# Optimization experiments

Measured on AMD Instinct MI355X. Metric: run time of the kernel, lower is better.

The kernel has to match this reference:

```python
import jax, jax.numpy as jnp
import numpy as np

B, T, C, HS = 256, 256, 384, 64

def setup_inputs() -> dict:
    key = jax.random.key(0)
    k1, k2, k3, k4 = jax.random.split(key, 4)
    s = 1.0 / np.sqrt(C)  # Linear-like init scale
    return {
        "x": jax.random.normal(k1, (B, T, C), dtype=jnp.float32),
        "Wq": jax.random.normal(k2, (C, HS), dtype=jnp.float32) * s,
        "Wk": jax.random.normal(k3, (C, HS), dtype=jnp.float32) * s,
        "Wv": jax.random.normal(k4, (C, HS), dtype=jnp.float32) * s,
    }

def reference(x, Wq, Wk, Wv):
    # q,k,v: [B,T,HS]
    q = jnp.einsum("btc,ch->bth", x, Wq)
    k = jnp.einsum("btc,ch->bth", x, Wk)
    v = jnp.einsum("btc,ch->bth", x, Wv)
    scale = k.shape[-1] ** -0.5
    scores = jnp.einsum("bth,bsh->bts", q, k) * scale  # [B,T,T]
    causal = jnp.tril(jnp.ones((x.shape[1], x.shape[1]), dtype=bool))
    scores = jnp.where(causal, scores, -jnp.inf)
    attn = jax.nn.softmax(scores, axis=-1)
    # dropout omitted (eval mode / deterministic reference)
    return jnp.einsum("bts,bsh->bth", attn, v)
```

## Files before the change

kernel.cpp:

```cpp
#include <hip/hip_runtime.h>
#include <hip/hip_bf16.h>

#define NB 256
#define NT 256
#define NC 384
#define NH 64
#define NW 192
#define WT_ELEMS (NW * NC)

typedef short bf16x8 __attribute__((ext_vector_type(8)));
typedef float f32x4 __attribute__((ext_vector_type(4)));

__device__ __forceinline__ unsigned short f2bf(float f) {
  union { float f; unsigned int i; } c;
  c.f = f;
  const unsigned int r = c.i + 0x7fffu + ((c.i >> 16) & 1u);
  return (unsigned short)(r >> 16);
}

__device__ __forceinline__ unsigned short f2bf_hw(float f) {
  __hip_bfloat16 b = __float2bfloat16(f);
  return *reinterpret_cast<unsigned short*>(&b);
}

__device__ __forceinline__ bf16x8 cvt8(float4 lo, float4 hi) {
  union { bf16x8 v; unsigned short u[8]; } au;
  au.u[0] = f2bf_hw(lo.x); au.u[1] = f2bf_hw(lo.y);
  au.u[2] = f2bf_hw(lo.z); au.u[3] = f2bf_hw(lo.w);
  au.u[4] = f2bf_hw(hi.x); au.u[5] = f2bf_hw(hi.y);
  au.u[6] = f2bf_hw(hi.z); au.u[7] = f2bf_hw(hi.w);
  return au.v;
}

__global__ __launch_bounds__(256) void w_prep_kernel(
    const float* __restrict__ Wq,
    const float* __restrict__ Wk,
    const float* __restrict__ Wv,
    unsigned short* __restrict__ Wt2) {
  const int o = blockIdx.x * 256 + threadIdx.x;
  if (o >= WT_ELEMS) return;
  const int j = o & 7;
  const int lane = (o >> 3) & 63;
  const int fi = o >> 9;
  const int ni = fi % 12;
  const int kt = fi / 12;
  const int n = ni * 16 + (lane & 15);
  const int k = kt * 32 + ((lane >> 4) << 3) + j;
  const float* W = (n < 64) ? Wq : (n < 128) ? Wk : Wv;
  Wt2[o] = f2bf(W[k * NH + (n & 63)]);
}

__global__ __launch_bounds__(1024, 4) void fused_qkv_attn_kernel(
    const float* __restrict__ x,
    const unsigned short* __restrict__ Wt2,
    float* __restrict__ out) {
  __shared__ __align__(16) unsigned char lds[147456];

  const int tid = threadIdx.x;
  const int w = tid >> 6;
  const int lane = tid & 63;
  const int l15 = lane & 15;
  const int lg = lane >> 4;
  const int b = blockIdx.x;
  const int row0 = b * NT;
  const int qt =
      (int)((0x583E2F49C1A7B6D0ull >> (w << 2)) & 15ull);
  const int wbase = qt * 16;

  f32x4 acc[12];
#pragma unroll
  for (int ni = 0; ni < 12; ++ni)
#pragma unroll
    for (int r = 0; r < 4; ++r) acc[ni][r] = 0.f;

#pragma unroll
  for (int i = 0; i < 9; ++i) {
    const int idx = i * 1024 + tid;
    __builtin_amdgcn_global_load_lds(
        (const __attribute__((address_space(1))) void*)(Wt2 + idx * 8),
        (__attribute__((address_space(3))) void*)(lds + idx * 16), 16, 0, 0);
  }

  const float* xa0 = x + (size_t)(row0 + wbase + l15) * NC + lg * 8;

  float4 aA0, aA1, aB0, aB1, aC0, aC1;

#define LOADA(S, KT)                                                          \
  do {                                                                        \
    a##S##0 = *reinterpret_cast<const float4*>(xa0 + (KT)*32);                \
    a##S##1 = *reinterpret_cast<const float4*>(xa0 + (KT)*32 + 4);            \
  } while (0)

  LOADA(A, 0);
  LOADA(B, 1);
  LOADA(C, 2);

  asm volatile("s_waitcnt vmcnt(0)" ::: "memory");
  __builtin_amdgcn_s_barrier();

  const unsigned short* Wl =
      reinterpret_cast<const unsigned short*>(lds) + lane * 8;

#define STEP(S, KT)                                                           \
  do {                                                                        \
    const bf16x8 afr = cvt8(a##S##0, a##S##1);                                \
    if ((KT) + 3 < 12) LOADA(S, (KT) + 3);                                    \
    _Pragma("unroll") for (int ni = 0; ni < 12; ++ni) {                       \
      const bf16x8 bfr = *reinterpret_cast<const bf16x8*>(                    \
          Wl + (size_t)((KT)*12 + ni) * 512);                                 \
      acc[ni] = __builtin_amdgcn_mfma_f32_16x16x32_bf16(                      \
          afr, bfr, acc[ni], 0, 0, 0);                                        \
    }                                                                         \
  } while (0)

  STEP(A, 0);  STEP(B, 1);  STEP(C, 2);
  STEP(A, 3);  STEP(B, 4);  STEP(C, 5);
  STEP(A, 6);  STEP(B, 7);  STEP(C, 8);
  STEP(A, 9);  STEP(B, 10); STEP(C, 11);

  __syncthreads();

  unsigned short* Kls = reinterpret_cast<unsigned short*>(lds);
  unsigned short* Vtls = reinterpret_cast<unsigned short*>(lds + 32768);
  unsigned short* Qls = reinterpret_cast<unsigned short*>(lds + 65536);
  unsigned short* Pls = reinterpret_cast<unsigned short*>(lds + 98304);

#pragma unroll
  for (int ni = 0; ni < 12; ++ni) {
    const int n = ni * 16 + l15;
#pragma unroll
    for (int r = 0; r < 4; ++r) {
      const int srow = wbase + lg * 4 + r;
      const unsigned short val = f2bf_hw(acc[ni][r]);
      if (ni < 4) {
        Qls[srow * 64 + (n ^ ((srow & 7) << 3))] = val;
      } else if (ni < 8) {
        const int h = n - 64;
        Kls[srow * 64 + (h ^ ((srow & 7) << 3))] = val;
      } else {
        const int h = n - 128;
        Vtls[h * 256 + (srow ^ ((h & 7) << 3))] = val;
      }
    }
  }
  __syncthreads();

  bf16x8 a_q[2];
#pragma unroll
  for (int ks = 0; ks < 2; ++ks) {
    const int srow = wbase + l15;
    a_q[ks] = *reinterpret_cast<const bf16x8*>(
        Qls + srow * 64 + ((ks * 32 + lg * 8) ^ ((srow & 7) << 3)));
  }

  f32x4 o[4];
  float mrun[4], lrun[4];
#pragma unroll
  for (int r = 0; r < 4; ++r) {
    mrun[r] = -3.0e38f;
    lrun[r] = 0.f;
#pragma unroll
    for (int hi = 0; hi < 4; ++hi) o[hi][r] = 0.f;
  }

  unsigned short* Pw = Pls + w * 640;
  const int njmax = qt >> 1;

  for (int j = 0; j <= njmax; ++j) {
    f32x4 s_acc[2];
#pragma unroll
    for (int si = 0; si < 2; ++si)
#pragma unroll
      for (int r = 0; r < 4; ++r) s_acc[si][r] = 0.f;

#pragma unroll
    for (int ks = 0; ks < 2; ++ks) {
      bf16x8 bk[2];
#pragma unroll
      for (int si = 0; si < 2; ++si) {
        const int srow = j * 32 + si * 16 + l15;
        const int kel = ks * 32 + lg * 8;
        bk[si] = *reinterpret_cast<const bf16x8*>(
            Kls + srow * 64 + (kel ^ ((srow & 7) << 3)));
      }
#pragma unroll
      for (int si = 0; si < 2; ++si)
        s_acc[si] = __builtin_amdgcn_mfma_f32_16x16x32_bf16(
            a_q[ks], bk[si], s_acc[si], 0, 0, 0);
    }

    const bool dlast = (j == njmax);
#pragma unroll
    for (int r = 0; r < 4; ++r) {
      const int mloc = lg * 4 + r;
      float v0 = s_acc[0][r] * 0.125f;
      float v1 = s_acc[1][r] * 0.125f;
      if (dlast) {
        if ((qt & 1) == 0) {
          if (l15 > mloc) v0 = -3.0e38f;
          v1 = -3.0e38f;
        } else {
          if (l15 > mloc) v1 = -3.0e38f;
        }
      }
      float pm = fmaxf(v0, v1);
      pm = fmaxf(pm, __shfl_xor(pm, 1, 16));
      pm = fmaxf(pm, __shfl_xor(pm, 2, 16));
      pm = fmaxf(pm, __shfl_xor(pm, 4, 16));
      pm = fmaxf(pm, __shfl_xor(pm, 8, 16));
      const float mnew = fmaxf(mrun[r], pm);
      const float alpha = __expf(mrun[r] - mnew);
      mrun[r] = mnew;
      const float p0 = __expf(v0 - mnew);
      const float p1 = __expf(v1 - mnew);
      float ps = p0 + p1;
      ps += __shfl_xor(ps, 1, 16);
      ps += __shfl_xor(ps, 2, 16);
      ps += __shfl_xor(ps, 4, 16);
      ps += __shfl_xor(ps, 8, 16);
      lrun[r] = lrun[r] * alpha + ps;
#pragma unroll
      for (int hi = 0; hi < 4; ++hi) o[hi][r] *= alpha;
      Pw[mloc * 40 + l15] = f2bf(p0);
      Pw[mloc * 40 + 16 + l15] = f2bf(p1);
    }

    const bf16x8 pa =
        *reinterpret_cast<const bf16x8*>(Pw + l15 * 40 + lg * 8);
#pragma unroll
    for (int hi = 0; hi < 4; ++hi) {
      const int h = hi * 16 + l15;
      const int sel = j * 32 + lg * 8;
      const bf16x8 bv = *reinterpret_cast<const bf16x8*>(
          Vtls + h * 256 + (sel ^ ((h & 7) << 3)));
      o[hi] = __builtin_amdgcn_mfma_f32_16x16x32_bf16(pa, bv, o[hi], 0, 0, 0);
    }
  }

  float* og = out + ((size_t)b * NT + wbase) * NH;
#pragma unroll
  for (int r = 0; r < 4; ++r) {
    const float inv = 1.f / lrun[r];
    const int m = lg * 4 + r;
#pragma unroll
    for (int hi = 0; hi < 4; ++hi)
      og[m * 64 + hi * 16 + l15] = o[hi][r] * inv;
  }
}

extern "C" void kernel_launch(void* const* d_in, const int* in_sizes, int n_in,
                              void* d_out, int out_size, void* d_ws,
                              size_t ws_size, hipStream_t stream) {
  const float* x  = (const float*)d_in[0];
  const float* Wq = (const float*)d_in[1];
  const float* Wk = (const float*)d_in[2];
  const float* Wv = (const float*)d_in[3];
  unsigned short* Wt2 = (unsigned short*)d_ws;
  float* out = (float*)d_out;

  w_prep_kernel<<<dim3((WT_ELEMS + 255) / 256), dim3(256), 0, stream>>>(
      Wq, Wk, Wv, Wt2);
  fused_qkv_attn_kernel<<<dim3(NB), dim3(1024), 0, stream>>>(x, Wt2, out);
}
```

Before: 41.04 us.

## Retile QKV projection as 32x96 per wave to reuse weight fragments

Each wave now computes a 32-row by 96-column block of the QKV projection instead of a 16-row by 192-column strip. Every weight fragment read from LDS now feeds two MFMAs, which halves LDS traffic for B operands. The x prefetch pipeline drops from three stages to two to fit the doubled A registers. The row-to-wave assignment for the attention phase is decoupled and recomputed after the barrier. The cost is more live vector registers per lane, which may pressure occupancy.

```diff
diff --git a/kernel.cpp b/kernel.cpp
--- a/kernel.cpp
+++ b/kernel.cpp
@@ -63,15 +63,16 @@
   const int lg = lane >> 4;
   const int b = blockIdx.x;
   const int row0 = b * NT;
-  const int qt =
-      (int)((0x583E2F49C1A7B6D0ull >> (w << 2)) & 15ull);
-  const int wbase = qt * 16;
-
-  f32x4 acc[12];
-#pragma unroll
-  for (int ni = 0; ni < 12; ++ni)
-#pragma unroll
-    for (int r = 0; r < 4; ++r) acc[ni][r] = 0.f;
+  const int rg = w >> 1;
+  const int ch = w & 1;
+
+  f32x4 acc[2][6];
+#pragma unroll
+  for (int mi = 0; mi < 2; ++mi)
+#pragma unroll
+    for (int ni = 0; ni < 6; ++ni)
+#pragma unroll
+      for (int r = 0; r < 4; ++r) acc[mi][ni][r] = 0.f;
 
 #pragma unroll
   for (int i = 0; i < 9; ++i) {
@@ -81,19 +82,21 @@
         (__attribute__((address_space(3))) void*)(lds + idx * 16), 16, 0, 0);
   }
 
-  const float* xa0 = x + (size_t)(row0 + wbase + l15) * NC + lg * 8;
-
-  float4 aA0, aA1, aB0, aB1, aC0, aC1;
+  const float* xa0 = x + (size_t)(row0 + rg * 32 + l15) * NC + lg * 8;
+  const float* xa1 = xa0 + (size_t)16 * NC;
+
+  float4 aA0, aA1, aA2, aA3, aB0, aB1, aB2, aB3;
 
 #define LOADA(S, KT)                                                          \
   do {                                                                        \
     a##S##0 = *reinterpret_cast<const float4*>(xa0 + (KT)*32);                \
     a##S##1 = *reinterpret_cast<const float4*>(xa0 + (KT)*32 + 4);            \
+    a##S##2 = *reinterpret_cast<const float4*>(xa1 + (KT)*32);                \
+    a##S##3 = *reinterpret_cast<const float4*>(xa1 + (KT)*32 + 4);            \
   } while (0)
 
   LOADA(A, 0);
   LOADA(B, 1);
-  LOADA(C, 2);
 
   asm volatile("s_waitcnt vmcnt(0)" ::: "memory");
   __builtin_amdgcn_s_barrier();
@@ -101,22 +104,27 @@
   const unsigned short* Wl =
       reinterpret_cast<const unsigned short*>(lds) + lane * 8;
 
-#define STEP(S, KT)                                                           \
-  do {                                                                        \
-    const bf16x8 afr = cvt8(a##S##0, a##S##1);                                \
-    if ((KT) + 3 < 12) LOADA(S, (KT) + 3);                                    \
-    _Pragma("unroll") for (int ni = 0; ni < 12; ++ni) {                       \
-      const bf16x8 bfr = *reinterpret_cast<const bf16x8*>(                    \
-          Wl + (size_t)((KT)*12 + ni) * 512);                                 \
-      acc[ni] = __builtin_amdgcn_mfma_f32_16x16x32_bf16(                      \
-          afr, bfr, acc[ni], 0, 0, 0);                                        \
-    }                                                                         \
+#define STEP(S, KT)                                                          \
+  do {                                                                       \
+    const bf16x8 afr0 = cvt8(a##S##0, a##S##1);                              \
+    const bf16x8 afr1 = cvt8(a##S##2, a##S##3);                              \
+    if ((KT) + 2 < 12) LOADA(S, (KT) + 2);                                   \
+    _Pragma("unroll") for (int ni = 0; ni < 6; ++ni) {                       \
+      const bf16x8 bfr = *reinterpret_cast<const bf16x8*>(                   \
+          Wl + (size_t)((KT)*12 + ch * 6 + ni) * 512);                       \
+      acc[0][ni] = __builtin_amdgcn_mfma_f32_16x16x32_bf16(                  \
+          afr0, bfr, acc[0][ni], 0, 0, 0);                                   \
+      acc[1][ni] = __builtin_amdgcn_mfma_f32_16x16x32_bf16(                  \
+          afr1, bfr, acc[1][ni], 0, 0, 0);                                   \
+    }                                                                        \
   } while (0)
 
-  STEP(A, 0);  STEP(B, 1);  STEP(C, 2);
-  STEP(A, 3);  STEP(B, 4);  STEP(C, 5);
-  STEP(A, 6);  STEP(B, 7);  STEP(C, 8);
-  STEP(A, 9);  STEP(B, 10); STEP(C, 11);
+  STEP(A, 0);  STEP(B, 1);
+  STEP(A, 2);  STEP(B, 3);
+  STEP(A, 4);  STEP(B, 5);
+  STEP(A, 6);  STEP(B, 7);
+  STEP(A, 8);  STEP(B, 9);
+  STEP(A, 10); STEP(B, 11);
 
   __syncthreads();
 
@@ -126,24 +134,29 @@
   unsigned short* Pls = reinterpret_cast<unsigned short*>(lds + 98304);
 
 #pragma unroll
-  for (int ni = 0; ni < 12; ++ni) {
-    const int n = ni * 16 + l15;
-#pragma unroll
-    for (int r = 0; r < 4; ++r) {
-      const int srow = wbase + lg * 4 + r;
-      const unsigned short val = f2bf_hw(acc[ni][r]);
-      if (ni < 4) {
-        Qls[srow * 64 + (n ^ ((srow & 7) << 3))] = val;
-      } else if (ni < 8) {
-        const int h = n - 64;
-        Kls[srow * 64 + (h ^ ((srow & 7) << 3))] = val;
-      } else {
-        const int h = n - 128;
-        Vtls[h * 256 + (srow ^ ((h & 7) << 3))] = val;
+  for (int mi = 0; mi < 2; ++mi)
+#pragma unroll
+    for (int ni = 0; ni < 6; ++ni) {
+      const int n = ch * 96 + ni * 16 + l15;
+#pragma unroll
+      for (int r = 0; r < 4; ++r) {
+        const int srow = rg * 32 + mi * 16 + lg * 4 + r;
+        const unsigned short val = f2bf_hw(acc[mi][ni][r]);
+        if (n < 64) {
+          Qls[srow * 64 + (n ^ ((srow & 7) << 3))] = val;
+        } else if (n < 128) {
+          const int h = n - 64;
+          Kls[srow * 64 + (h ^ ((srow & 7) << 3))] = val;
+        } else {
+          const int h = n - 128;
+          Vtls[h * 256 + (srow ^ ((h & 7) << 3))] = val;
+        }
       }
     }
-  }
   __syncthreads();
+
+  const int qt = (int)((0x583E2F49C1A7B6D0ull >> (w << 2)) & 15ull);
+  const int wbase = qt * 16;
 
   bf16x8 a_q[2];
 #pragma unroll
```

New measurement: 49.49 us. +20.6%, slower.
